# Kernel optimization log

Hardware: AMD Instinct MI355X
Metric: run time of the kernel (lower is better)

Reference implementation:

```python
import jax, jax.numpy as jnp
import numpy as np

B, T, IN, OUT = 4, 2048, 4096, 11008


def setup_inputs() -> dict:
    key = jax.random.key(0)
    k1, k2, k3, k4 = jax.random.split(key, 4)
    x = jax.random.normal(k1, (B, T, IN), dtype=jnp.float32)
    # int8 weight values in [-127, 127]; stored as int32 for harness dtype support
    weight_int8 = jax.random.randint(k2, (OUT, IN), -127, 128, dtype=jnp.int32)
    # per-output-channel scales, positive and small like absmax/127
    weight_scale = jax.random.uniform(k3, (OUT, 1), dtype=jnp.float32, minval=1e-4, maxval=0.02)
    bias = jax.random.normal(k4, (OUT,), dtype=jnp.float32) * 0.01
    return {"x": x, "weight_int8": weight_int8, "weight_scale": weight_scale, "bias": bias}


def reference(x, weight_int8, weight_scale, bias):
    # dequantize: [OUT, IN] float weight = int8 * per-row scale
    weight_fp = weight_int8.astype(jnp.float32) * weight_scale
    weight_fp = weight_fp.astype(x.dtype)
    # F.linear: x @ W^T + b -> [B, T, OUT]
    out = jnp.einsum('bti,oi->bto', x, weight_fp) + bias
    return out
```

## Files before the change

### kernel.cpp

```cpp
#include <hip/hip_runtime.h>
#include <hip/hip_bf16.h>

#define MDIM 8192
#define NDIM 11008
#define KDIM 4096

#define BM 256
#define BN 256
#define BK 64
#define NT (KDIM / BK)

typedef __attribute__((ext_vector_type(4))) int int4v;


__global__ __launch_bounds__(256) void quant_x_kernel(const float* __restrict__ x,
                                                      int* __restrict__ q,
                                                      float* __restrict__ xs) {
  int row = blockIdx.x;
  int tid = threadIdx.x;
  const float4* xr = (const float4*)(x + (size_t)row * KDIM);
  float4 v[4];
  float amax = 0.f;
#pragma unroll
  for (int i = 0; i < 4; ++i) {
    v[i] = xr[tid + i * 256];
    amax = fmaxf(amax, fmaxf(fmaxf(fabsf(v[i].x), fabsf(v[i].y)),
                             fmaxf(fabsf(v[i].z), fabsf(v[i].w))));
  }
#pragma unroll
  for (int off = 32; off; off >>= 1)
    amax = fmaxf(amax, __shfl_xor(amax, off));
  __shared__ float smax[4];
  if ((tid & 63) == 0) smax[tid >> 6] = amax;
  __syncthreads();
  amax = fmaxf(fmaxf(smax[0], smax[1]), fmaxf(smax[2], smax[3]));
  amax = fmaxf(amax, 1e-20f);
  float inv = 127.f / amax;
  if (tid == 0) xs[row] = amax * (1.f / 127.f);
  int* qr = q + (size_t)row * (KDIM / 4);
#pragma unroll
  for (int i = 0; i < 4; ++i) {
    int a = (int)rintf(v[i].x * inv) & 255;
    int b = (int)rintf(v[i].y * inv) & 255;
    int c = (int)rintf(v[i].z * inv) & 255;
    int d = (int)rintf(v[i].w * inv);
    qr[tid + i * 256] = a | (b << 8) | (c << 16) | (d << 24);
  }
}


__global__ void cvt_w_kernel(const int* __restrict__ w, int* __restrict__ q, int n) {
  int stride = gridDim.x * blockDim.x;
  for (int i = blockIdx.x * blockDim.x + threadIdx.x; i < n; i += stride) {
    int4v v = *(const int4v*)(w + (size_t)i * 4);
    q[i] = (v.x & 255) | ((v.y & 255) << 8) | ((v.z & 255) << 16) | (v.w << 24);
  }
}


#define SBARR() __builtin_amdgcn_sched_barrier(0)
#define BARR()  __builtin_amdgcn_s_barrier()
#define VMW_(n) asm volatile("s_waitcnt vmcnt(" #n ")" ::: "memory")
#define VMW(n)  VMW_(n)

#define GLL(SRC, DST) \
  __builtin_amdgcn_global_load_lds( \
      (const __attribute__((address_space(1))) void*)(SRC), \
      (__attribute__((address_space(3))) void*)(DST), 16, 0, 0)

#define STAGE(GSRC, LBASE, BUFI, T) do { \
    const char* _s = (GSRC) + (T) * 64; \
    GLL(_s, (LBASE) + (BUFI) * 16384 + w * 1024); \
    GLL(_s + rstep, (LBASE) + (BUFI) * 16384 + w * 1024 + 8192); \
  } while (0)

#define RD(LB, BUFI, ROW) \
  (*(const int4v*)((LB) + (BUFI) * 16384 + (ROW) * 64 + kbs))

#define MFMA16(AF, MOFF) do { \
    _Pragma("unroll") for (int mi = 0; mi < 4; ++mi) \
    _Pragma("unroll") for (int ni = 0; ni < 4; ++ni) \
      acc[(MOFF) + mi][ni] = __builtin_amdgcn_mfma_i32_16x16x64_i8( \
          af[mi], bf[ni], acc[(MOFF) + mi][ni], 0, 0, 0); \
  } while (0)

#define KT(T, B_, SD, TAIL) do { \
    _Pragma("unroll") for (int ni = 0; ni < 4; ++ni) bf[ni] = RD(ldsB, B_, brow0 + ni * 16); \
    _Pragma("unroll") for (int mi = 0; mi < 4; ++mi) af[mi] = RD(ldsA, B_, arow0 + mi * 16); \
    if (SD) STAGE(gAs, ldsA, (B_) ^ 1, (T) + 1); \
    SBARR(); \
    __builtin_amdgcn_s_setprio(1); MFMA16(af, 0); __builtin_amdgcn_s_setprio(0); \
    SBARR(); \
    _Pragma("unroll") for (int mi = 0; mi < 4; ++mi) af[mi] = RD(ldsA, B_, arow0 + 64 + mi * 16); \
    if (SD) STAGE(gBs, ldsB, (B_) ^ 1, (T) + 1); \
    SBARR(); \
    __builtin_amdgcn_s_setprio(1); MFMA16(af, 4); __builtin_amdgcn_s_setprio(0); \
    SBARR(); \
    if (!(TAIL)) { VMW(0); BARR(); SBARR(); } \
  } while (0)

__global__ __launch_bounds__(512, 2) void gemm_i8_kernel(
    const char* __restrict__ A,
    const char* __restrict__ Bt,
    const float* __restrict__ xs,
    const float* __restrict__ scale,
    const float* __restrict__ bias,
    float* __restrict__ C)
{
  __shared__ __attribute__((aligned(16))) char As[2][256][64];
  __shared__ __attribute__((aligned(16))) char Bs[2][256][64];

  int bid = blockIdx.x;
  int cpx = gridDim.x >> 3;
  int swz = (bid & 7) * cpx + (bid >> 3);
  int srow = swz / 344;
  int rem  = swz - srow * 344;
  int scol, q;
  if (rem < 320) { scol = rem >> 5; q = rem & 31; }
  else           { scol = 10;       q = rem - 320; }
  int brow = (srow * 8 + (q & 7)) * BM;
  int bcol = (scol * 4 + (q >> 3)) * BN;

  int tid  = threadIdx.x;
  int lane = tid & 63;
  int w    = tid >> 6;
  int wr   = (w >> 2) & 1;
  int wc   = w & 3;

  int ra = lane & 15;
  int kb = (lane >> 4) * 16;
  int kbs = kb ^ (((ra >> 1) & 3) << 4);

  int arow0 = wr * 128 + ra;
  int brow0 = wc * 64 + ra;

  int srw = w * 16 + (lane >> 2);
  int csrc = (lane & 3) ^ ((lane >> 3) & 3);
  const char* gAs = A  + (size_t)(brow + srw) * KDIM + csrc * 16;
  const char* gBs = Bt + (size_t)(bcol + srw) * KDIM + csrc * 16;
  const size_t rstep = (size_t)128 * KDIM;

  char* ldsA = &As[0][0][0];
  char* ldsB = &Bs[0][0][0];

  int4v acc[8][4] = {};
  int4v af[4], bf[4];

  STAGE(gAs, ldsA, 0, 0);  STAGE(gBs, ldsB, 0, 0);
  VMW(0); BARR(); SBARR();

  for (int t = 0; t < 62; t += 2) {
    KT(t,     0, 1, 0);
    KT(t + 1, 1, 1, 0);
  }
  KT(62, 0, 1, 0);
  KT(63, 1, 0, 1);

  int col0 = bcol + wc * 64 + ra;
  int row0 = brow + wr * 128 + (lane >> 4) * 4;
  float xr_[8][4];
#pragma unroll
  for (int m = 0; m < 8; ++m)
#pragma unroll
    for (int j = 0; j < 4; ++j)
      xr_[m][j] = xs[row0 + m * 16 + j];
#pragma unroll
  for (int n = 0; n < 4; ++n) {
    int ng = col0 + n * 16;
    float sc = scale[ng];
    float bi = bias[ng];
#pragma unroll
    for (int m = 0; m < 8; ++m) {
      int rg = row0 + m * 16;
#pragma unroll
      for (int j = 0; j < 4; ++j)
        __builtin_nontemporal_store((float)acc[m][n][j] * (xr_[m][j] * sc) + bi,
                                    &C[(size_t)(rg + j) * NDIM + ng]);
    }
  }
}


__global__ void naive_kernel(const float* __restrict__ x, const int* __restrict__ w,
                             const float* __restrict__ scale, const float* __restrict__ bias,
                             float* __restrict__ out)
{
  int n = blockIdx.x * blockDim.x + threadIdx.x;
  int m = blockIdx.y;
  if (n >= NDIM) return;
  const float* xr = x + (size_t)m * KDIM;
  const int* wrow = w + (size_t)n * KDIM;
  float s = 0.f;
  for (int k = 0; k < KDIM; ++k) s += xr[k] * (float)wrow[k];
  out[(size_t)m * NDIM + n] = s * scale[n] + bias[n];
}


extern "C" void kernel_launch(void* const* d_in, const int* in_sizes, int n_in,
                              void* d_out, int out_size, void* d_ws, size_t ws_size,
                              hipStream_t stream) {
  const float* x      = (const float*)d_in[0];
  const int*   w8     = (const int*)d_in[1];
  const float* wscale = (const float*)d_in[2];
  const float* bias   = (const float*)d_in[3];
  float* out = (float*)d_out;

  size_t aq = (size_t)MDIM * KDIM;
  size_t bq = (size_t)NDIM * KDIM;
  size_t xb = (size_t)MDIM * 4;

  if (ws_size >= aq + bq + xb) {
    char* Aq = (char*)d_ws;
    char* Bq = (char*)d_ws + aq;
    float* xsp = (float*)((char*)d_ws + aq + bq);
    quant_x_kernel<<<MDIM, 256, 0, stream>>>(x, (int*)Aq, xsp);
    cvt_w_kernel<<<2048, 256, 0, stream>>>(w8, (int*)Bq, NDIM * KDIM / 4);
    gemm_i8_kernel<<<(MDIM / BM) * (NDIM / BN), 512, 0, stream>>>(
        Aq, Bq, xsp, wscale, bias, out);
  } else {
    naive_kernel<<<dim3((NDIM + 255) / 256, MDIM), 256, 0, stream>>>(x, w8, wscale, bias, out);
  }
}
```

Before: 490.4 us.

## Shrink M tile to 128 and use triple-buffered LDS pipeline for int8 GEMM

Halves the block M tile to 128 rows, so each wave accumulates a 64x64 output and the accumulator register count drops. The LDS pipeline goes from double to triple buffering, prefetching two k-steps ahead and waiting with a partial vmcnt instead of draining all loads each step. The block swizzle is reworked for twice as many row tiles. The intent is to hide global-load latency and reduce register pressure, at the cost of lower arithmetic intensity per block and more total global traffic.

```diff
diff --git a/kernel.cpp b/kernel.cpp
--- a/kernel.cpp
+++ b/kernel.cpp
@@ -5,7 +5,7 @@
 #define NDIM 11008
 #define KDIM 4096
 
-#define BM 256
+#define BM 128
 #define BN 256
 #define BK 64
 #define NT (KDIM / BK)
@@ -68,35 +68,29 @@
       (const __attribute__((address_space(1))) void*)(SRC), \
       (__attribute__((address_space(3))) void*)(DST), 16, 0, 0)
 
-#define STAGE(GSRC, LBASE, BUFI, T) do { \
-    const char* _s = (GSRC) + (T) * 64; \
-    GLL(_s, (LBASE) + (BUFI) * 16384 + w * 1024); \
-    GLL(_s + rstep, (LBASE) + (BUFI) * 16384 + w * 1024 + 8192); \
+#define STAGE_A(BUFI, T) \
+  GLL(gAs + (T) * 64, ldsA + (BUFI) * 8192 + w * 1024)
+#define STAGE_B(BUFI, T) do { \
+    GLL(gBs + (T) * 64,         ldsB + (BUFI) * 16384 + w * 1024); \
+    GLL(gBs + (T) * 64 + rstep, ldsB + (BUFI) * 16384 + 8192 + w * 1024); \
   } while (0)
 
-#define RD(LB, BUFI, ROW) \
-  (*(const int4v*)((LB) + (BUFI) * 16384 + (ROW) * 64 + kbs))
-
-#define MFMA16(AF, MOFF) do { \
+#define RDA(BUFI, ROW) (*(const int4v*)(ldsA + (BUFI) * 8192  + (ROW) * 64 + kbs))
+#define RDB(BUFI, ROW) (*(const int4v*)(ldsB + (BUFI) * 16384 + (ROW) * 64 + kbs))
+
+#define KT(T, SLT, SS, SD, VN, TAIL) do { \
+    _Pragma("unroll") for (int ni = 0; ni < 4; ++ni) bf[ni] = RDB(SLT, brow0 + ni * 16); \
+    _Pragma("unroll") for (int mi = 0; mi < 4; ++mi) af[mi] = RDA(SLT, arow0 + mi * 16); \
+    if (SD) { STAGE_A(SS, (T) + 2); STAGE_B(SS, (T) + 2); } \
+    SBARR(); \
+    __builtin_amdgcn_s_setprio(1); \
     _Pragma("unroll") for (int mi = 0; mi < 4; ++mi) \
     _Pragma("unroll") for (int ni = 0; ni < 4; ++ni) \
-      acc[(MOFF) + mi][ni] = __builtin_amdgcn_mfma_i32_16x16x64_i8( \
-          af[mi], bf[ni], acc[(MOFF) + mi][ni], 0, 0, 0); \
-  } while (0)
-
-#define KT(T, B_, SD, TAIL) do { \
-    _Pragma("unroll") for (int ni = 0; ni < 4; ++ni) bf[ni] = RD(ldsB, B_, brow0 + ni * 16); \
-    _Pragma("unroll") for (int mi = 0; mi < 4; ++mi) af[mi] = RD(ldsA, B_, arow0 + mi * 16); \
-    if (SD) STAGE(gAs, ldsA, (B_) ^ 1, (T) + 1); \
+      acc[mi][ni] = __builtin_amdgcn_mfma_i32_16x16x64_i8( \
+          af[mi], bf[ni], acc[mi][ni], 0, 0, 0); \
+    __builtin_amdgcn_s_setprio(0); \
     SBARR(); \
-    __builtin_amdgcn_s_setprio(1); MFMA16(af, 0); __builtin_amdgcn_s_setprio(0); \
-    SBARR(); \
-    _Pragma("unroll") for (int mi = 0; mi < 4; ++mi) af[mi] = RD(ldsA, B_, arow0 + 64 + mi * 16); \
-    if (SD) STAGE(gBs, ldsB, (B_) ^ 1, (T) + 1); \
-    SBARR(); \
-    __builtin_amdgcn_s_setprio(1); MFMA16(af, 4); __builtin_amdgcn_s_setprio(0); \
-    SBARR(); \
-    if (!(TAIL)) { VMW(0); BARR(); SBARR(); } \
+    if (!(TAIL)) { VMW(VN); BARR(); SBARR(); } \
   } while (0)
 
 __global__ __launch_bounds__(512, 2) void gemm_i8_kernel(
@@ -107,35 +101,36 @@
     const float* __restrict__ bias,
     float* __restrict__ C)
 {
-  __shared__ __attribute__((aligned(16))) char As[2][256][64];
-  __shared__ __attribute__((aligned(16))) char Bs[2][256][64];
+  __shared__ __attribute__((aligned(16))) char As[3][128][64];
+  __shared__ __attribute__((aligned(16))) char Bs[3][256][64];
 
   int bid = blockIdx.x;
   int cpx = gridDim.x >> 3;
   int swz = (bid & 7) * cpx + (bid >> 3);
-  int srow = swz / 344;
-  int rem  = swz - srow * 344;
+  int band = swz / 688;
+  int rem  = swz - band * 688;
   int scol, q;
-  if (rem < 320) { scol = rem >> 5; q = rem & 31; }
-  else           { scol = 10;       q = rem - 320; }
-  int brow = (srow * 8 + (q & 7)) * BM;
-  int bcol = (scol * 4 + (q >> 3)) * BN;
+  if (rem < 640) { scol = rem >> 6;  q = rem & 63; }
+  else           { scol = 10;        q = rem - 640; }
+  int brow, bcol;
+  if (rem < 640) { brow = (band * 16 + (q & 15)) * BM; bcol = (scol * 4 + (q >> 4)) * BN; }
+  else           { brow = (band * 16 + (q & 15)) * BM; bcol = (40 + (q >> 4)) * BN; }
 
   int tid  = threadIdx.x;
   int lane = tid & 63;
   int w    = tid >> 6;
-  int wr   = (w >> 2) & 1;
+  int wr   = w >> 2;
   int wc   = w & 3;
 
   int ra = lane & 15;
   int kb = (lane >> 4) * 16;
   int kbs = kb ^ (((ra >> 1) & 3) << 4);
 
-  int arow0 = wr * 128 + ra;
+  int arow0 = wr * 64 + ra;
   int brow0 = wc * 64 + ra;
 
-  int srw = w * 16 + (lane >> 2);
-  int csrc = (lane & 3) ^ ((lane >> 3) & 3);
+  int srw  = tid >> 2;
+  int csrc = (tid & 3) ^ ((tid >> 3) & 3);
   const char* gAs = A  + (size_t)(brow + srw) * KDIM + csrc * 16;
   const char* gBs = Bt + (size_t)(bcol + srw) * KDIM + csrc * 16;
   const size_t rstep = (size_t)128 * KDIM;
@@ -143,39 +138,38 @@
   char* ldsA = &As[0][0][0];
   char* ldsB = &Bs[0][0][0];
 
-  int4v acc[8][4] = {};
+  int4v acc[4][4] = {};
   int4v af[4], bf[4];
 
-  STAGE(gAs, ldsA, 0, 0);  STAGE(gBs, ldsB, 0, 0);
-  VMW(0); BARR(); SBARR();
-
-  for (int t = 0; t < 62; t += 2) {
-    KT(t,     0, 1, 0);
-    KT(t + 1, 1, 1, 0);
-  }
-  KT(62, 0, 1, 0);
-  KT(63, 1, 0, 1);
+  STAGE_A(0, 0);  STAGE_B(0, 0);
+  STAGE_A(1, 1);  STAGE_B(1, 1);
+  VMW(3); BARR(); SBARR();
+
+  for (int t = 0; t < 60; t += 3) {
+    KT(t,     0, 2, 1, 3, 0);
+    KT(t + 1, 1, 0, 1, 3, 0);
+    KT(t + 2, 2, 1, 1, 3, 0);
+  }
+  KT(60, 0, 2, 1, 3, 0);
+  KT(61, 1, 0, 1, 3, 0);
+  KT(62, 2, 0, 0, 0, 0);
+  KT(63, 0, 0, 0, 0, 1);
 
   int col0 = bcol + wc * 64 + ra;
-  int row0 = brow + wr * 128 + (lane >> 4) * 4;
-  float xr_[8][4];
-#pragma unroll
-  for (int m = 0; m < 8; ++m)
-#pragma unroll
-    for (int j = 0; j < 4; ++j)
-      xr_[m][j] = xs[row0 + m * 16 + j];
+  int row0 = brow + wr * 64 + (lane >> 4) * 4;
 #pragma unroll
   for (int n = 0; n < 4; ++n) {
     int ng = col0 + n * 16;
     float sc = scale[ng];
     float bi = bias[ng];
 #pragma unroll
-    for (int m = 0; m < 8; ++m) {
+    for (int m = 0; m < 4; ++m) {
       int rg = row0 + m * 16;
 #pragma unroll
       for (int j = 0; j < 4; ++j)
-        __builtin_nontemporal_store((float)acc[m][n][j] * (xr_[m][j] * sc) + bi,
-                                    &C[(size_t)(rg + j) * NDIM + ng]);
+        __builtin_nontemporal_store(
+            (float)acc[m][n][j] * (xs[rg + j] * sc) + bi,
+            &C[(size_t)(rg + j) * NDIM + ng]);
     }
   }
 }
```

New measurement: 564.3 us. 15.1% more time.

## Deepen int8 GEMM LDS pipeline to four buffers with quadrant-split MFMA phases

Applied to the files above, without the earlier changes.

Expands the LDS ring from two to four stages and prefetches two k-tiles ahead, so global loads have more time to land before use. Each k-tile is split into four 8-MFMA phases that reuse A/B fragment halves, with each staged global-to-LDS load interleaved between phases and separated by barriers and lgkmcnt waits. It aims to hide global memory latency and spread LDS traffic, but doubles LDS use to 128KB per block, which at launch_bounds(512,2) may cut occupancy or exceed LDS capacity. It also adds many extra workgroup barriers per k-tile.

```diff
diff --git a/kernel.cpp b/kernel.cpp
--- a/kernel.cpp
+++ b/kernel.cpp
@@ -60,6 +60,7 @@
 
 #define SBARR() __builtin_amdgcn_sched_barrier(0)
 #define BARR()  __builtin_amdgcn_s_barrier()
+#define LGK0()  asm volatile("s_waitcnt lgkmcnt(0)" ::: "memory")
 #define VMW_(n) asm volatile("s_waitcnt vmcnt(" #n ")" ::: "memory")
 #define VMW(n)  VMW_(n)
 
@@ -68,35 +69,49 @@
       (const __attribute__((address_space(1))) void*)(SRC), \
       (__attribute__((address_space(3))) void*)(DST), 16, 0, 0)
 
-#define STAGE(GSRC, LBASE, BUFI, T) do { \
-    const char* _s = (GSRC) + (T) * 64; \
-    GLL(_s, (LBASE) + (BUFI) * 16384 + w * 1024); \
-    GLL(_s + rstep, (LBASE) + (BUFI) * 16384 + w * 1024 + 8192); \
+#define STAGE_A_LO(BUFI, T) GLL(gAs + (T) * 64,         ldsA + (BUFI) * 16384 + w * 1024)
+#define STAGE_A_HI(BUFI, T) GLL(gAs + (T) * 64 + rstep, ldsA + (BUFI) * 16384 + 8192 + w * 1024)
+#define STAGE_B_LO(BUFI, T) GLL(gBs + (T) * 64,         ldsB + (BUFI) * 16384 + w * 1024)
+#define STAGE_B_HI(BUFI, T) GLL(gBs + (T) * 64 + rstep, ldsB + (BUFI) * 16384 + 8192 + w * 1024)
+
+#define RDA(BUFI, ROW) (*(const int4v*)(ldsA + (BUFI) * 16384 + (ROW) * 64 + kbs))
+#define RDB(BUFI, ROW) (*(const int4v*)(ldsB + (BUFI) * 16384 + (ROW) * 64 + kbs))
+
+#define MFMA8(AF, BF, MH, NH) do { \
+    _Pragma("unroll") for (int mi = 0; mi < 4; ++mi) \
+    _Pragma("unroll") for (int ni = 0; ni < 2; ++ni) \
+      acc[(MH) * 4 + mi][(NH) * 2 + ni] = __builtin_amdgcn_mfma_i32_16x16x64_i8( \
+          AF[mi], BF[ni], acc[(MH) * 4 + mi][(NH) * 2 + ni], 0, 0, 0); \
   } while (0)
 
-#define RD(LB, BUFI, ROW) \
-  (*(const int4v*)((LB) + (BUFI) * 16384 + (ROW) * 64 + kbs))
-
-#define MFMA16(AF, MOFF) do { \
-    _Pragma("unroll") for (int mi = 0; mi < 4; ++mi) \
-    _Pragma("unroll") for (int ni = 0; ni < 4; ++ni) \
-      acc[(MOFF) + mi][ni] = __builtin_amdgcn_mfma_i32_16x16x64_i8( \
-          af[mi], bf[ni], acc[(MOFF) + mi][ni], 0, 0, 0); \
-  } while (0)
-
-#define KT(T, B_, SD, TAIL) do { \
-    _Pragma("unroll") for (int ni = 0; ni < 4; ++ni) bf[ni] = RD(ldsB, B_, brow0 + ni * 16); \
-    _Pragma("unroll") for (int mi = 0; mi < 4; ++mi) af[mi] = RD(ldsA, B_, arow0 + mi * 16); \
-    if (SD) STAGE(gAs, ldsA, (B_) ^ 1, (T) + 1); \
+#define KTILE(T, SLT, SD, DW, VN, LAST) do { \
+    const int _ss = ((SLT) + 2) & 3; \
+     \
+    _Pragma("unroll") for (int mi = 0; mi < 4; ++mi) afL[mi] = RDA(SLT, arow0 + mi * 16); \
+    bfL[0] = RDB(SLT, brow0);      bfL[1] = RDB(SLT, brow0 + 16); \
+    if (SD) STAGE_A_LO(_ss, (T) + 2); \
+    SBARR(); BARR(); LGK0(); SBARR(); \
+    __builtin_amdgcn_s_setprio(1); MFMA8(afL, bfL, 0, 0); __builtin_amdgcn_s_setprio(0); \
+    SBARR(); BARR(); SBARR(); \
+     \
+    bfH[0] = RDB(SLT, brow0 + 32); bfH[1] = RDB(SLT, brow0 + 48); \
+    if (SD) STAGE_A_HI(_ss, (T) + 2); \
+    SBARR(); BARR(); LGK0(); SBARR(); \
+    __builtin_amdgcn_s_setprio(1); MFMA8(afL, bfH, 0, 1); __builtin_amdgcn_s_setprio(0); \
+    SBARR(); BARR(); SBARR(); \
+     \
+    _Pragma("unroll") for (int mi = 0; mi < 4; ++mi) afH[mi] = RDA(SLT, arow0 + 64 + mi * 16); \
+    if (SD) STAGE_B_LO(_ss, (T) + 2); \
+    SBARR(); BARR(); LGK0(); SBARR(); \
+    __builtin_amdgcn_s_setprio(1); MFMA8(afH, bfH, 1, 1); __builtin_amdgcn_s_setprio(0); \
+    SBARR(); BARR(); SBARR(); \
+     \
+    if (SD) STAGE_B_HI(_ss, (T) + 2); \
+    SBARR(); BARR(); LGK0(); SBARR(); \
+    __builtin_amdgcn_s_setprio(1); MFMA8(afH, bfL, 1, 0); __builtin_amdgcn_s_setprio(0); \
     SBARR(); \
-    __builtin_amdgcn_s_setprio(1); MFMA16(af, 0); __builtin_amdgcn_s_setprio(0); \
-    SBARR(); \
-    _Pragma("unroll") for (int mi = 0; mi < 4; ++mi) af[mi] = RD(ldsA, B_, arow0 + 64 + mi * 16); \
-    if (SD) STAGE(gBs, ldsB, (B_) ^ 1, (T) + 1); \
-    SBARR(); \
-    __builtin_amdgcn_s_setprio(1); MFMA16(af, 4); __builtin_amdgcn_s_setprio(0); \
-    SBARR(); \
-    if (!(TAIL)) { VMW(0); BARR(); SBARR(); } \
+    if (DW) { VMW(VN); } \
+    if (!(LAST)) { BARR(); SBARR(); } \
   } while (0)
 
 __global__ __launch_bounds__(512, 2) void gemm_i8_kernel(
@@ -107,8 +122,8 @@
     const float* __restrict__ bias,
     float* __restrict__ C)
 {
-  __shared__ __attribute__((aligned(16))) char As[2][256][64];
-  __shared__ __attribute__((aligned(16))) char Bs[2][256][64];
+  __shared__ __attribute__((aligned(16))) char As[4][256][64];
+  __shared__ __attribute__((aligned(16))) char Bs[4][256][64];
 
   int bid = blockIdx.x;
   int cpx = gridDim.x >> 3;
@@ -144,17 +159,22 @@
   char* ldsB = &Bs[0][0][0];
 
   int4v acc[8][4] = {};
-  int4v af[4], bf[4];
-
-  STAGE(gAs, ldsA, 0, 0);  STAGE(gBs, ldsB, 0, 0);
-  VMW(0); BARR(); SBARR();
-
-  for (int t = 0; t < 62; t += 2) {
-    KT(t,     0, 1, 0);
-    KT(t + 1, 1, 1, 0);
-  }
-  KT(62, 0, 1, 0);
-  KT(63, 1, 0, 1);
+  int4v afL[4], afH[4], bfL[2], bfH[2];
+
+  STAGE_A_LO(0, 0); STAGE_A_HI(0, 0); STAGE_B_LO(0, 0); STAGE_B_HI(0, 0);
+  STAGE_A_LO(1, 1); STAGE_A_HI(1, 1); STAGE_B_LO(1, 1); STAGE_B_HI(1, 1);
+  VMW(4); BARR(); SBARR();
+
+  for (int t = 0; t < 60; t += 4) {
+    KTILE(t,     0, 1, 1, 4, 0);
+    KTILE(t + 1, 1, 1, 1, 4, 0);
+    KTILE(t + 2, 2, 1, 1, 4, 0);
+    KTILE(t + 3, 3, 1, 1, 4, 0);
+  }
+  KTILE(60, 0, 1, 1, 4, 0);
+  KTILE(61, 1, 1, 1, 4, 0);
+  KTILE(62, 2, 0, 1, 0, 0);
+  KTILE(63, 3, 0, 0, 0, 1);
 
   int col0 = bcol + wc * 64 + ra;
   int row0 = brow + wr * 128 + (lane >> 4) * 4;
```

Result: slower. 506.8 us (+3.3%).
